# Kernel optimization log

Measured on AMD Instinct MI355X. Metric: run time of the kernel, lower is better.

The kernel has to match this reference:

```python
import jax, jax.numpy as jnp
import numpy as np
import math

B, N, HORIZON, E = 16, 4096, 12, 16
IN_DIM = HORIZON * E            # 192
T_DIM, H, D = 64, 4, 16         # transformer_dim, heads, head_dim
K_ORD = 3
FFN = 128
OUT_DIM = HORIZON * 16          # horizon * dim_out = 192
LN_EPS = 1e-5


def setup_inputs() -> dict:
    key = jax.random.key(0)
    ks = jax.random.split(key, 16)
    s = 0.02
    return {
        "x": jax.random.normal(ks[0], (B, N, IN_DIM), jnp.float32),
        "Wq": jax.random.normal(ks[1], (IN_DIM, T_DIM), jnp.float32) * s,
        "bq": jnp.zeros((T_DIM,), jnp.float32),
        "Wk": jax.random.normal(ks[2], (IN_DIM, T_DIM), jnp.float32) * s,
        "bk": jnp.zeros((T_DIM,), jnp.float32),
        "Wv": jax.random.normal(ks[3], (IN_DIM, T_DIM), jnp.float32) * s,
        "bv": jnp.zeros((T_DIM,), jnp.float32),
        "Win": jax.random.normal(ks[4], (IN_DIM, T_DIM), jnp.float32) * s,  # no bias
        "Wout": jax.random.normal(ks[5], (T_DIM, OUT_DIM), jnp.float32) * s,
        "bout": jnp.zeros((OUT_DIM,), jnp.float32),
        "W1": jax.random.normal(ks[6], (T_DIM, FFN), jnp.float32) * s,
        "b1": jnp.zeros((FFN,), jnp.float32),
        "W2": jax.random.normal(ks[7], (FFN, T_DIM), jnp.float32) * s,
        "b2": jnp.zeros((T_DIM,), jnp.float32),
        "ln_g": jnp.ones((T_DIM,), jnp.float32),
        "ln_b": jnp.zeros((T_DIM,), jnp.float32),
        "weights_pool": jax.random.normal(ks[8], (IN_DIM, OUT_DIM), jnp.float32) * s,
        "Pi": jax.random.normal(ks[9], (H, K_ORD + 1), jnp.float32) * 0.5,
    }


def _layer_norm(y, g, b):
    mu = jnp.mean(y, axis=-1, keepdims=True)
    var = jnp.mean((y - mu) ** 2, axis=-1, keepdims=True)
    return (y - mu) * jax.lax.rsqrt(var + LN_EPS) * g + b


def reference(x, Wq, bq, Wk, bk, Wv, bv, Win, Wout, bout,
              W1, b1, W2, b2, ln_g, ln_b, weights_pool, Pi):
    Bx, Nx, _ = x.shape
    # projections -> (B, H, N, d)
    Q = (x @ Wq + bq).reshape(Bx, Nx, H, D).transpose(0, 2, 1, 3)
    Kt = (x @ Wk + bk).reshape(Bx, Nx, H, D).transpose(0, 2, 1, 3)
    V = (x @ Wv + bv).reshape(Bx, Nx, H, D).transpose(0, 2, 1, 3)

    weighted_sum = jnp.zeros((Bx, H, Nx, D), x.dtype)
    for k in range(K_ORD + 1):
        if k == 0:
            # transform(0, .) returns ones with feature dim 1
            Qk = jnp.ones((Bx, H, Nx, 1), x.dtype)
            Kk = jnp.ones((Bx, H, Nx, 1), x.dtype)
        else:
            Qk = Q ** k   # elementwise power (exp-by-squaring == x**k)
            Kk = Kt ** k
        dk = Qk.shape[-1]
        # f_kv: (B,H,f,d) ; sumN: (B,H,f,1)
        f_kv = jnp.einsum('bhnf,bhnc->bhfc', Kk, V)
        sumN = jnp.sum(Kk, axis=2)[..., None]
        f_kv_norm = f_kv / (sumN + 1e-8) / math.sqrt(dk)
        c_k = jnp.einsum('bhnf,bhfc->bhnc', Qk, f_kv_norm)
        weighted_sum = weighted_sum + c_k * Pi[:, k][None, :, None, None]

    # NOTE: faithful to original: raw view of (B,H,N,d) as (B,N,H*d), no permute
    attention_out = weighted_sum.reshape(Bx, Nx, H * D) / math.factorial(K_ORD)

    proj = x @ Win
    res = _layer_norm(proj + attention_out, ln_g, ln_b)
    ffn = jax.nn.relu(res @ W1 + b1) @ W2 + b2   # dropout = identity (eval)
    res = _layer_norm(res + ffn, ln_g, ln_b)

    x_g = jnp.einsum('bni,io->bno', x, weights_pool)
    out = res @ Wout + bout
    return x_g + out
```

## Files before the change

kernel.cpp:

```cpp
#include <hip/hip_runtime.h>

typedef unsigned int u32;
typedef unsigned short u16;

#define NB 16
#define NN 4096
#define IND 192

typedef __attribute__((ext_vector_type(8))) short short8;
typedef __attribute__((ext_vector_type(4))) float f32x4;
#define MFMA16 __builtin_amdgcn_mfma_f32_16x16x32_bf16

__device__ __forceinline__ float bf2f(u16 u) {
  union { u32 i; float f; } c; c.i = ((u32)u) << 16; return c.f;
}
__device__ __forceinline__ float lo16(u32 u) {
  union { u32 i; float f; } c; c.i = u << 16; return c.f;
}
__device__ __forceinline__ float hi16(u32 u) {
  union { u32 i; float f; } c; c.i = u & 0xffff0000u; return c.f;
}
__device__ __forceinline__ u16 f2bf(float f) {
  union { float f; u32 i; } c; c.f = f;
  u32 r = c.i + 0x7fffu + ((c.i >> 16) & 1u);
  return (u16)(r >> 16);
}
__device__ __forceinline__ float ldwf(const void* p, int i, int isf) {
  return isf ? ((const float*)p)[i] : bf2f(((const u16*)p)[i]);
}
__device__ __forceinline__ short8 ld_frag8(const u16* p) {
  union { uint4 u; short8 s; } c;
  c.u = *reinterpret_cast<const uint4*>(p);
  return c.s;
}
__device__ __forceinline__ short8 as_short8(uint4 u) {
  union { uint4 u; short8 s; } c; c.u = u; return c.s;
}
__device__ __forceinline__ short8 pack8(const float* v) {
  short8 s;
  #pragma unroll
  for (int e = 0; e < 8; ++e) s[e] = (short)f2bf(v[e]);
  return s;
}
__device__ __forceinline__ float ln64(float y, float g, float be) {
  float s = y, sq = y * y;
  #pragma unroll
  for (int off = 32; off > 0; off >>= 1) {
    s  += __shfl_xor(s, off, 64);
    sq += __shfl_xor(sq, off, 64);
  }
  float mu  = s * 0.015625f;
  float var = sq * 0.015625f - mu * mu;
  return (y - mu) * rsqrtf(var + 1e-5f) * g + be;
}

__global__ __launch_bounds__(64) void k_detect(const u32* __restrict__ x2,
                                               int* __restrict__ flag) {
  int t = threadIdx.x;
  int bad = 0;
  for (int i = 0; i < 16; ++i) {
    float a = fabsf(lo16(x2[t * 16 + i]));
    if (!(a < 1e4f)) bad = 1;
  }
  int anybad = __any(bad);
  if (t == 0) *flag = anybad ? 1 : 0;
}

__global__ __launch_bounds__(256) void k_xb(const int* __restrict__ flag,
                                            const void* __restrict__ x,
                                            u16* __restrict__ xb) {
  const int isf = *flag;
  size_t gid = (size_t)blockIdx.x * 256 + threadIdx.x;
  if (isf) {
    const float4* src = (const float4*)x;
    for (size_t i = gid; i < 3145728; i += 1048576) {
      float4 v = src[i];
      ushort4 o;
      o.x = f2bf(v.x); o.y = f2bf(v.y); o.z = f2bf(v.z); o.w = f2bf(v.w);
      ((ushort4*)xb)[i] = o;
    }
  } else {
    const uint4* src = (const uint4*)x;
    for (size_t i = gid; i < 1572864; i += 1048576)
      ((uint4*)xb)[i] = src[i];
  }
}

__global__ __launch_bounds__(192) void k_xsum(const int* __restrict__ flag,
                                              const void* __restrict__ x,
                                              float* __restrict__ xsum) {
  const int isf = *flag;
  const int t = threadIdx.x;
  const int r0 = blockIdx.x * 256;
  const int b = r0 >> 12;
  float s = 0.f;
  if (isf) {
    const float* xp = (const float*)x;
    for (int r = 0; r < 256; ++r) s += xp[(size_t)(r0 + r) * 192 + t];
  } else {
    const u16* xp = (const u16*)x;
    for (int r = 0; r < 256; ++r) s += bf2f(xp[(size_t)(r0 + r) * 192 + t]);
  }
  atomicAdd(xsum + b * 192 + t, s);
}

__global__ __launch_bounds__(256) void k_prepw(
    const int* __restrict__ flag,
    const void* Wq, const void* Wk, const void* Wv, const void* Win,
    const void* Wout, const void* Wp, const void* W1, const void* W2,
    const void* bq, const void* bk, const void* bv,
    u16* __restrict__ Bs1, u16* __restrict__ BsKlo, u16* __restrict__ Bs2,
    u16* __restrict__ W1f, u16* __restrict__ W2f, float* __restrict__ bcat)
{
  const int isf = *flag;
  int idx = blockIdx.x * 256 + threadIdx.x;
  if (idx < 49152) {
    int e = idx & 7, l = (idx >> 3) & 63, g = idx >> 9;
    int nt = g & 15, ks = g >> 4;
    int k = ks * 32 + (l >> 4) * 8 + e;
    int n = nt * 16 + (l & 15);
    const void* W = (n < 64) ? Wq : (n < 128) ? Wk : (n < 192) ? Wv : Win;
    Bs1[idx] = f2bf(ldwf(W, k * 64 + (n & 63), isf));
  } else if (idx < 61440) {
    int j = idx - 49152;
    int e = j & 7, l = (j >> 3) & 63, g = j >> 9;
    int ntp = g & 3, ks = g >> 2;
    int k = ks * 32 + (l >> 4) * 8 + e;
    int n = ntp * 16 + (l & 15);
    float wv = ldwf(Wk, k * 64 + n, isf);
    u16 hi = f2bf(wv);
    BsKlo[j] = f2bf(wv - bf2f(hi));
  } else if (idx < 110592) {
    int j = idx - 61440;
    int e = j & 7, l = (j >> 3) & 63, g = j >> 9;
    int nt = g % 12, ks = g / 12;
    int k = ks * 32 + (l >> 4) * 8 + e;
    int n = nt * 16 + (l & 15);
    float v = (k < 64) ? ldwf(Wout, k * 192 + n, isf)
                       : ldwf(Wp, (k - 64) * 192 + n, isf);
    Bs2[j] = f2bf(v);
  } else if (idx < 118784) {
    int j = idx - 110592;
    int e = j & 7, l = (j >> 3) & 63, g = j >> 9;
    int nt = g & 7, ks = g >> 3;
    int k = ks * 32 + (l >> 4) * 8 + e;
    int n = nt * 16 + (l & 15);
    W1f[j] = f2bf(ldwf(W1, k * 128 + n, isf));
  } else if (idx < 126976) {
    int j = idx - 118784;
    int e = j & 7, l = (j >> 3) & 63, g = j >> 9;
    int nt = g & 3, ks = g >> 2;
    int k = ks * 32 + (l >> 4) * 8 + e;
    int n = nt * 16 + (l & 15);
    W2f[j] = f2bf(ldwf(W2, k * 64 + n, isf));
  } else if (idx < 127232) {
    int n = idx - 126976;
    bcat[n] = (n < 64)  ? ldwf(bq, n, isf)
            : (n < 128) ? ldwf(bk, n - 64, isf)
            : (n < 192) ? ldwf(bv, n - 128, isf) : 0.f;
  }
}

template<bool F32>
__device__ void gemm1_body(const void* __restrict__ x,
                           const u16* __restrict__ Bs1,
                           const u16* __restrict__ BsKlo,
                           const float* __restrict__ bcat,
                           u16* __restrict__ C1, float* __restrict__ stats,
                           float (*xs)[196], float (*Ks)[65], float (*Vs)[65])
{
  const int tid = threadIdx.x;
  const int mbase = blockIdx.x * 32;
  const int b = mbase >> 12;

  if constexpr (F32) {
    for (int i = tid; i < 1536; i += 512) {
      int row = i / 48, c4 = i - row * 48;
      float4 v = *((const float4*)x + (size_t)(mbase + row) * 48 + c4);
      *(float4*)&xs[row][c4 * 4] = v;
    }
  } else {
    for (int i = tid; i < 768; i += 512) {
      int row = i / 24, c8 = i - row * 24;
      uint4 v = *((const uint4*)x + (size_t)(mbase + row) * 24 + c8);
      float* dst = &xs[row][c8 * 8];
      dst[0]=lo16(v.x); dst[1]=hi16(v.x); dst[2]=lo16(v.y); dst[3]=hi16(v.y);
      dst[4]=lo16(v.z); dst[5]=hi16(v.z); dst[6]=lo16(v.w); dst[7]=hi16(v.w);
    }
  }
  __syncthreads();

  const int w = tid >> 6, l = tid & 63, lm = l & 15, lk = l >> 4;
  const int nt0 = w * 2;
  const bool isK = (w == 2) || (w == 3);

  short8 bhi[2][6], blo[2][6];
  #pragma unroll
  for (int n2 = 0; n2 < 2; ++n2)
    #pragma unroll
    for (int ks = 0; ks < 6; ++ks) {
      bhi[n2][ks] = ld_frag8(Bs1 + (size_t)((ks * 16 + nt0 + n2) * 64 + l) * 8);
      if (F32 && isK)
        blo[n2][ks] = ld_frag8(BsKlo + (size_t)((ks * 4 + nt0 + n2 - 4) * 64 + l) * 8);
    }
  float bias[2];
  bias[0] = bcat[nt0 * 16 + lm];
  bias[1] = bcat[(nt0 + 1) * 16 + lm];

  for (int mt = 0; mt < 2; ++mt) {
    short8 ahi[6], alo[6];
    const float* xr = &xs[mt * 16 + lm][0];
    #pragma unroll
    for (int ks = 0; ks < 6; ++ks) {
      float v[8];
      *(float4*)&v[0] = *(const float4*)(xr + ks * 32 + lk * 8);
      *(float4*)&v[4] = *(const float4*)(xr + ks * 32 + lk * 8 + 4);
      short8 h8;
      #pragma unroll
      for (int e = 0; e < 8; ++e) h8[e] = (short)f2bf(v[e]);
      ahi[ks] = h8;
      if (F32 && isK) {
        short8 l8;
        #pragma unroll
        for (int e = 0; e < 8; ++e) {
          float r = v[e] - bf2f((u16)h8[e]);
          l8[e] = (short)f2bf(r);
        }
        alo[ks] = l8;
      }
    }
    f32x4 acc[2];
    #pragma unroll
    for (int n2 = 0; n2 < 2; ++n2) {
      f32x4 a = {bias[n2], bias[n2], bias[n2], bias[n2]};
      acc[n2] = a;
    }
    #pragma unroll
    for (int ks = 0; ks < 6; ++ks)
      #pragma unroll
      for (int n2 = 0; n2 < 2; ++n2) {
        acc[n2] = MFMA16(ahi[ks], bhi[n2][ks], acc[n2], 0, 0, 0);
        if (F32 && isK) {
          acc[n2] = MFMA16(ahi[ks], blo[n2][ks], acc[n2], 0, 0, 0);
          acc[n2] = MFMA16(alo[ks], bhi[n2][ks], acc[n2], 0, 0, 0);
          acc[n2] = MFMA16(alo[ks], blo[n2][ks], acc[n2], 0, 0, 0);
        }
      }
    const int rl = mt * 16 + lk * 4;
    if (w < 2) {
      #pragma unroll
      for (int n2 = 0; n2 < 2; ++n2)
        #pragma unroll
        for (int r = 0; r < 4; ++r)
          C1[(size_t)(mbase + rl + r) * 128 + (nt0 + n2) * 16 + lm] = f2bf(acc[n2][r]);
    } else if (isK) {
      #pragma unroll
      for (int n2 = 0; n2 < 2; ++n2)
        #pragma unroll
        for (int r = 0; r < 4; ++r)
          Ks[rl + r][(nt0 + n2 - 4) * 16 + lm] = acc[n2][r];
    } else if (w < 6) {
      #pragma unroll
      for (int n2 = 0; n2 < 2; ++n2)
        #pragma unroll
        for (int r = 0; r < 4; ++r)
          Vs[rl + r][(nt0 + n2 - 8) * 16 + lm] = acc[n2][r];
    } else {
      #pragma unroll
      for (int n2 = 0; n2 < 2; ++n2)
        #pragma unroll
        for (int r = 0; r < 4; ++r)
          C1[(size_t)(mbase + rl + r) * 128 + 64 + (nt0 + n2 - 12) * 16 + lm] = f2bf(acc[n2][r]);
    }
  }
  __syncthreads();

  float* sb = stats + (size_t)(b * 4) * 832;
  #pragma unroll
  for (int it = 0; it < 2; ++it) {
    int item = tid + it * 512;
    int hh = item >> 8, f = (item >> 4) & 15, c = item & 15;
    float a1 = 0.f, a2 = 0.f, a3 = 0.f;
    for (int r = 0; r < 32; ++r) {
      float kv = Ks[r][hh * 16 + f];
      float vv = Vs[r][hh * 16 + c];
      float k2 = kv * kv;
      a1 = fmaf(kv, vv, a1);
      a2 = fmaf(k2, vv, a2);
      a3 = fmaf(k2 * kv, vv, a3);
    }
    float* base = sb + (size_t)hh * 832 + f * 16 + c;
    atomicAdd(base, a1);
    atomicAdd(base + 256, a2);
    atomicAdd(base + 512, a3);
  }
  if (tid < 192) {
    int kk = tid >> 6, hf = tid & 63, h2 = hf >> 4, ff = hf & 15;
    float s = 0.f;
    for (int r = 0; r < 32; ++r) {
      float kv = Ks[r][hf];
      s += (kk == 0) ? kv : (kk == 1) ? kv * kv : kv * kv * kv;
    }
    atomicAdd(sb + (size_t)h2 * 832 + 768 + kk * 16 + ff, s);
  } else if (tid < 256) {
    int hf = tid - 192, h2 = hf >> 4;
    float s = 0.f;
    for (int r = 0; r < 32; ++r) s += Vs[r][hf];
    atomicAdd(sb + (size_t)h2 * 832 + 816 + (hf & 15), s);
  }
}

__global__ __launch_bounds__(512, 2) void k_gemm1(
    const int* __restrict__ flag, const void* __restrict__ x,
    const u16* __restrict__ Bs1, const u16* __restrict__ BsKlo,
    const float* __restrict__ bcat,
    u16* __restrict__ C1, float* __restrict__ stats)
{
  __shared__ float xs[32][196];
  __shared__ float Ks[32][65];
  __shared__ float Vs[32][65];
  if (*flag) gemm1_body<true >(x, Bs1, BsKlo, bcat, C1, stats, xs, Ks, Vs);
  else       gemm1_body<false>(x, Bs1, BsKlo, bcat, C1, stats, xs, Ks, Vs);
}

template<bool F32>
__device__ void finalize_body(const float* stats, const void* Pi,
                              const void* Wk, const void* bk,
                              const float* xsum, float* M, float* sn1)
{
  const int bh = blockIdx.x, bb = bh >> 2, h = bh & 3, t = threadIdx.x;
  const float* sb = stats + (size_t)bh * 832;
  float* mb = M + (size_t)bh * 784;
  const float inv6 = 1.0f / 6.0f;

  {
    int f = t >> 4, s = t & 15;
    float p = 0.f;
    for (int i = s * 12; i < s * 12 + 12; ++i)
      p += xsum[bb * 192 + i] * ldwf(Wk, i * 64 + h * 16 + f, F32);
    p += __shfl_xor(p, 1, 64);
    p += __shfl_xor(p, 2, 64);
    p += __shfl_xor(p, 4, 64);
    p += __shfl_xor(p, 8, 64);
    if (s == 0) sn1[f] = p + 4096.0f * ldwf(bk, h * 16 + f, F32);
  }
  __syncthreads();

  {
    const int f = t >> 4, c = t & 15;
    #pragma unroll
    for (int k = 0; k < 3; ++k) {
      float fkv = sb[k * 256 + f * 16 + c];
      float sk  = (k == 0) ? sn1[f] : sb[768 + k * 16 + f];
      float pi  = ldwf(Pi, h * 4 + (k + 1), F32);
      mb[k * 256 + f * 16 + c] = fkv / ((sk + 1e-8f) * 4.0f) * pi * inv6;
    }
  }
  if (t < 16) {
    float sv  = sb[816 + t];
    float pi0 = ldwf(Pi, h * 4 + 0, F32);
    mb[768 + t] = sv / (4096.0f + 1e-8f) * pi0 * inv6;
  }
}

__global__ __launch_bounds__(256) void k_finalize(
    const int* __restrict__ flag, const float* __restrict__ stats,
    const void* __restrict__ Pi, const void* __restrict__ Wk,
    const void* __restrict__ bk, const float* __restrict__ xsum,
    float* __restrict__ M)
{
  __shared__ float sn1[16];
  if (*flag) finalize_body<true >(stats, Pi, Wk, bk, xsum, M, sn1);
  else       finalize_body<false>(stats, Pi, Wk, bk, xsum, M, sn1);
}

template<bool F32> __device__ void mid_body(
    const u16* __restrict__ C1, u16* __restrict__ R2,
    const float* __restrict__ Mall,
    const u16* __restrict__ W1f, const u16* __restrict__ W2f,
    const void* __restrict__ b1, const void* __restrict__ b2,
    const void* __restrict__ lng, const void* __restrict__ lnb,
    float (*attL)[72], u16 (*resB)[72], u16 (*hB)[136])
{
  const int tid = threadIdx.x;
  const int w = tid >> 6, l = tid & 63;
  const int lm = l & 15, lk = l >> 4;
  const int n0g = blockIdx.x * 64;
  const int b = n0g >> 12;
  const int n2_0 = n0g & 4095;
  const int h = n2_0 >> 10;
  const int qg0 = (b << 12) + ((n2_0 & 1023) << 2);
  const float* mb = Mall + (size_t)((b << 2) + h) * 784;

  short8 Bhi[2], Blo[2];
  #pragma unroll
  for (int ks = 0; ks < 2; ++ks) {
    float vh[8], vl[8];
    #pragma unroll
    for (int e = 0; e < 8; ++e) {
      int kk = ks * 32 + lk * 8 + e;
      float v = (kk < 16) ? mb[kk * 16 + lm]
              : (kk < 32) ? mb[256 + (kk - 16) * 16 + lm]
              : (kk < 48) ? mb[512 + (kk - 32) * 16 + lm] : 0.f;
      float hi = bf2f(f2bf(v));
      vh[e] = hi; vl[e] = v - hi;
    }
    Bhi[ks] = pack8(vh);
    Blo[ks] = pack8(vl);
  }
  const float c0v = mb[768 + lm];

  #pragma unroll
  for (int mt2 = 0; mt2 < 4; ++mt2) {
    const int mt = w * 4 + mt2;
    uint4 qv = *(const uint4*)(C1 + (size_t)(qg0 + mt * 16 + lm) * 128
                               + h * 16 + (lk & 1) * 8);
    float q[8] = {lo16(qv.x), hi16(qv.x), lo16(qv.y), hi16(qv.y),
                  lo16(qv.z), hi16(qv.z), lo16(qv.w), hi16(qv.w)};
    float q2[8], q3[8];
    #pragma unroll
    for (int e = 0; e < 8; ++e) { q2[e] = q[e] * q[e]; q3[e] = q2[e] * q[e]; }
    short8 a1, a2;
    if (lk < 2) { a1 = as_short8(qv); a2 = pack8(q3); }
    else        { a1 = pack8(q2);     a2 = short8{0,0,0,0,0,0,0,0}; }

    f32x4 acc = {c0v, c0v, c0v, c0v};
    acc = MFMA16(a1, Bhi[0], acc, 0, 0, 0);
    acc = MFMA16(a1, Blo[0], acc, 0, 0, 0);
    acc = MFMA16(a2, Bhi[1], acc, 0, 0, 0);
    acc = MFMA16(a2, Blo[1], acc, 0, 0, 0);

    #pragma unroll
    for (int r = 0; r < 4; ++r) {
      int qr = mt * 16 + lk * 4 + r;
      attL[qr >> 2][(qr & 3) * 16 + lm] = acc[r];
    }
  }

  const float gj = ldwf(lng, l, F32), bj = ldwf(lnb, l, F32);
  #pragma unroll 4
  for (int rr = 0; rr < 16; ++rr) {
    int r = w * 16 + rr;
    float proj = bf2f(C1[(size_t)(n0g + r) * 128 + 64 + l]);
    float y = proj + attL[r][l];
    resB[r][l] = f2bf(ln64(y, gj, bj));
  }

  short8 a0 = *(const short8*)&resB[w * 16 + lm][lk * 8];
  short8 a1f = *(const short8*)&resB[w * 16 + lm][32 + lk * 8];
  f32x4 hacc[8];
  #pragma unroll
  for (int nt = 0; nt < 8; ++nt) {
    float bv = ldwf(b1, nt * 16 + lm, F32);
    f32x4 a = {bv, bv, bv, bv};
    hacc[nt] = a;
  }
  #pragma unroll
  for (int nt = 0; nt < 8; ++nt) {
    short8 w1a = ld_frag8(W1f + (size_t)((0 * 8 + nt) * 64 + l) * 8);
    short8 w1b = ld_frag8(W1f + (size_t)((1 * 8 + nt) * 64 + l) * 8);
    hacc[nt] = MFMA16(a0, w1a, hacc[nt], 0, 0, 0);
    hacc[nt] = MFMA16(a1f, w1b, hacc[nt], 0, 0, 0);
  }
  #pragma unroll
  for (int nt = 0; nt < 8; ++nt)
    #pragma unroll
    for (int r = 0; r < 4; ++r) {
      int row = w * 16 + lk * 4 + r;
      hB[row][nt * 16 + lm] = f2bf(fmaxf(hacc[nt][r], 0.f));
    }

  short8 ha[4];
  #pragma unroll
  for (int ks = 0; ks < 4; ++ks)
    ha[ks] = *(const short8*)&hB[w * 16 + lm][ks * 32 + lk * 8];
  f32x4 oacc[4];
  #pragma unroll
  for (int nt = 0; nt < 4; ++nt) {
    float bv = ldwf(b2, nt * 16 + lm, F32);
    f32x4 a = {bv, bv, bv, bv};
    oacc[nt] = a;
  }
  #pragma unroll
  for (int ks = 0; ks < 4; ++ks)
    #pragma unroll
    for (int nt = 0; nt < 4; ++nt) {
      short8 w2v = ld_frag8(W2f + (size_t)((ks * 4 + nt) * 64 + l) * 8);
      oacc[nt] = MFMA16(ha[ks], w2v, oacc[nt], 0, 0, 0);
    }

  float gcol[4], bcol[4];
  #pragma unroll
  for (int nt = 0; nt < 4; ++nt) {
    gcol[nt] = ldwf(lng, nt * 16 + lm, F32);
    bcol[nt] = ldwf(lnb, nt * 16 + lm, F32);
  }
  #pragma unroll
  for (int r = 0; r < 4; ++r) {
    int row = w * 16 + lk * 4 + r;
    float y[4];
    float s = 0.f, sq = 0.f;
    #pragma unroll
    for (int nt = 0; nt < 4; ++nt) {
      y[nt] = oacc[nt][r] + bf2f(resB[row][nt * 16 + lm]);
      s += y[nt];
      sq = fmaf(y[nt], y[nt], sq);
    }
    #pragma unroll
    for (int off = 8; off > 0; off >>= 1) {
      s  += __shfl_xor(s, off, 64);
      sq += __shfl_xor(sq, off, 64);
    }
    float mu = s * 0.015625f;
    float var = sq * 0.015625f - mu * mu;
    float rs = rsqrtf(var + 1e-5f);
    #pragma unroll
    for (int nt = 0; nt < 4; ++nt) {
      float r2v = (y[nt] - mu) * rs * gcol[nt] + bcol[nt];
      R2[(size_t)(n0g + row) * 64 + nt * 16 + lm] = f2bf(r2v);
    }
  }
}

__global__ __launch_bounds__(256, 2) void k_mid(
    const int* __restrict__ flag, const u16* __restrict__ C1,
    u16* __restrict__ R2, const float* __restrict__ Mall,
    const u16* __restrict__ W1f, const u16* __restrict__ W2f,
    const void* __restrict__ b1, const void* __restrict__ b2,
    const void* __restrict__ lng, const void* __restrict__ lnb)
{
  __shared__ float attL[64][72];
  __shared__ u16 resB[64][72];
  __shared__ u16 hB[64][136];
  if (*flag) mid_body<true >(C1, R2, Mall, W1f, W2f, b1, b2, lng, lnb, attL, resB, hB);
  else       mid_body<false>(C1, R2, Mall, W1f, W2f, b1, b2, lng, lnb, attL, resB, hB);
}

__global__ __launch_bounds__(256, 2) void k_gemm2(
    const int* __restrict__ flag,
    const u16* __restrict__ R2, const u16* __restrict__ xb,
    const u16* __restrict__ Bs2, const void* __restrict__ bout,
    void* __restrict__ out)
{
  const int isf = *flag;
  const int l = threadIdx.x & 63;
  const int w = threadIdx.x >> 6;
  const int mbase = blockIdx.x * 64;
  const int lm = l & 15, lk = l >> 4;

  short8 bf[8][3];
  #pragma unroll
  for (int ks = 0; ks < 8; ++ks)
    #pragma unroll
    for (int nt = 0; nt < 3; ++nt)
      bf[ks][nt] = ld_frag8(Bs2 + (size_t)((ks * 12 + w * 3 + nt) * 64 + l) * 8);

  float bias[3];
  #pragma unroll
  for (int nt = 0; nt < 3; ++nt) bias[nt] = ldwf(bout, w * 48 + nt * 16 + lm, isf);

  short8 af[8];
  {
    const int row = mbase + lm;
    const u16* rp = R2 + (size_t)row * 64 + lk * 8;
    af[0] = ld_frag8(rp);
    af[1] = ld_frag8(rp + 32);
    const u16* xp = xb + (size_t)row * IND + lk * 8;
    #pragma unroll
    for (int ks = 2; ks < 8; ++ks) af[ks] = ld_frag8(xp + (ks - 2) * 32);
  }

  for (int mt = 0; mt < 4; ++mt) {
    short8 afn[8];
    if (mt < 3) {
      const int row = mbase + (mt + 1) * 16 + lm;
      const u16* rp = R2 + (size_t)row * 64 + lk * 8;
      afn[0] = ld_frag8(rp);
      afn[1] = ld_frag8(rp + 32);
      const u16* xp = xb + (size_t)row * IND + lk * 8;
      #pragma unroll
      for (int ks = 2; ks < 8; ++ks) afn[ks] = ld_frag8(xp + (ks - 2) * 32);
    }
    f32x4 acc[3];
    #pragma unroll
    for (int nt = 0; nt < 3; ++nt) {
      f32x4 a = {bias[nt], bias[nt], bias[nt], bias[nt]};
      acc[nt] = a;
    }
    #pragma unroll
    for (int ks = 0; ks < 8; ++ks)
      #pragma unroll
      for (int nt = 0; nt < 3; ++nt)
        acc[nt] = MFMA16(af[ks], bf[ks][nt], acc[nt], 0, 0, 0);
    const int r0 = mbase + mt * 16 + lk * 4;
    const int c0 = w * 48 + lm;
    if (isf) {
      float* op = (float*)out;
      #pragma unroll
      for (int nt = 0; nt < 3; ++nt)
        #pragma unroll
        for (int r = 0; r < 4; ++r)
          op[(size_t)(r0 + r) * IND + c0 + nt * 16] = acc[nt][r];
    } else {
      u16* op = (u16*)out;
      #pragma unroll
      for (int nt = 0; nt < 3; ++nt)
        #pragma unroll
        for (int r = 0; r < 4; ++r)
          op[(size_t)(r0 + r) * IND + c0 + nt * 16] = f2bf(acc[nt][r]);
    }
    #pragma unroll
    for (int ks = 0; ks < 8; ++ks) af[ks] = afn[ks];
  }
}

extern "C" void kernel_launch(void* const* d_in, const int* in_sizes, int n_in,
                              void* d_out, int out_size, void* d_ws, size_t ws_size,
                              hipStream_t stream)
{
  const void* x   = d_in[0];
  const void* Wq  = d_in[1];
  const void* bq  = d_in[2];
  const void* Wk  = d_in[3];
  const void* bk  = d_in[4];
  const void* Wv  = d_in[5];
  const void* bv  = d_in[6];
  const void* Win = d_in[7];
  const void* Wout= d_in[8];
  const void* bout= d_in[9];
  const void* W1  = d_in[10];
  const void* b1  = d_in[11];
  const void* W2  = d_in[12];
  const void* b2  = d_in[13];
  const void* lng = d_in[14];
  const void* lnb = d_in[15];
  const void* Wp  = d_in[16];
  const void* Pi  = d_in[17];

  u16* xb    = (u16*)d_ws;
  u16* C1    = xb + (size_t)12582912;
  u16* R2    = C1 + (size_t)8388608;
  u16* Bs1   = R2 + (size_t)4194304;
  u16* BsKlo = Bs1 + 49152;
  u16* Bs2   = BsKlo + 12288;
  u16* W1f   = Bs2 + 49152;
  u16* W2f   = W1f + 8192;
  float* bcat  = (float*)(W2f + 8192);
  float* stats = bcat + 256;
  float* xsum  = stats + 53248;
  float* Mc    = xsum + 3072;
  int*   flag  = (int*)(Mc + 50176);

  k_detect<<<1, 64, 0, stream>>>((const u32*)x, flag);
  hipMemsetAsync(stats, 0, (size_t)(53248 + 3072) * sizeof(float), stream);

  k_prepw<<<497, 256, 0, stream>>>(flag, Wq, Wk, Wv, Win, Wout, Wp, W1, W2,
                                   bq, bk, bv, Bs1, BsKlo, Bs2, W1f, W2f, bcat);
  k_xb<<<4096, 256, 0, stream>>>(flag, x, xb);
  k_xsum<<<256, 192, 0, stream>>>(flag, x, xsum);
  k_gemm1<<<2048, 512, 0, stream>>>(flag, x, Bs1, BsKlo, bcat, C1, stats);
  k_finalize<<<64, 256, 0, stream>>>(flag, stats, Pi, Wk, bk, xsum, Mc);
  k_mid<<<1024, 256, 0, stream>>>(flag, C1, R2, Mc, W1f, W2f, b1, b2, lng, lnb);
  k_gemm2<<<1024, 256, 0, stream>>>(flag, R2, xb, Bs2, bout, d_out);
}
```

Before: 161.5 us.

## Drop bf16 staging of x and restructure gemm1 with per-wave projection tiles

Removes the k_xb pass that wrote a bf16 copy of x; gemm1 and gemm2 now read x directly from global memory and convert fp32 to bf16 in registers. gemm1 is reorganised to 256 threads and 64 rows per block. Each wave computes one projection group with a block-rotated assignment, reading B fragments from global memory instead of holding them in registers, and the K-path error correction drops its lo*lo term. The K^kV statistics are register-blocked 4x4 per lane with shuffle reductions before fewer atomics, and k_xsum gets more, smaller blocks. This trades an extra full pass over x for re-reading fp32 x in gemm2 and repeated B-fragment loads.

```diff
diff --git a/kernel.cpp b/kernel.cpp
--- a/kernel.cpp
+++ b/kernel.cpp
@@ -16,9 +16,6 @@
 }
 __device__ __forceinline__ float lo16(u32 u) {
   union { u32 i; float f; } c; c.i = u << 16; return c.f;
-}
-__device__ __forceinline__ float hi16(u32 u) {
-  union { u32 i; float f; } c; c.i = u & 0xffff0000u; return c.f;
 }
 __device__ __forceinline__ u16 f2bf(float f) {
   union { float f; u32 i; } c; c.f = f;
@@ -33,15 +30,6 @@
   c.u = *reinterpret_cast<const uint4*>(p);
   return c.s;
 }
-__device__ __forceinline__ short8 as_short8(uint4 u) {
-  union { uint4 u; short8 s; } c; c.u = u; return c.s;
-}
-__device__ __forceinline__ short8 pack8(const float* v) {
-  short8 s;
-  #pragma unroll
-  for (int e = 0; e < 8; ++e) s[e] = (short)f2bf(v[e]);
-  return s;
-}
 __device__ __forceinline__ float ln64(float y, float g, float be) {
   float s = y, sq = y * y;
   #pragma unroll
@@ -52,6 +40,18 @@
   float mu  = s * 0.015625f;
   float var = sq * 0.015625f - mu * mu;
   return (y - mu) * rsqrtf(var + 1e-5f) * g + be;
+}
+__device__ __forceinline__ short8 pack8(const float* v) {
+  short8 s;
+  #pragma unroll
+  for (int e = 0; e < 8; ++e) s[e] = (short)f2bf(v[e]);
+  return s;
+}
+__device__ __forceinline__ short8 as_short8(uint4 u) {
+  union { uint4 u; short8 s; } c; c.u = u; return c.s;
+}
+__device__ __forceinline__ float hi16(u32 u) {
+  union { u32 i; float f; } c; c.i = u & 0xffff0000u; return c.f;
 }
 
 __global__ __launch_bounds__(64) void k_detect(const u32* __restrict__ x2,
@@ -66,40 +66,20 @@
   if (t == 0) *flag = anybad ? 1 : 0;
 }
 
-__global__ __launch_bounds__(256) void k_xb(const int* __restrict__ flag,
-                                            const void* __restrict__ x,
-                                            u16* __restrict__ xb) {
-  const int isf = *flag;
-  size_t gid = (size_t)blockIdx.x * 256 + threadIdx.x;
-  if (isf) {
-    const float4* src = (const float4*)x;
-    for (size_t i = gid; i < 3145728; i += 1048576) {
-      float4 v = src[i];
-      ushort4 o;
-      o.x = f2bf(v.x); o.y = f2bf(v.y); o.z = f2bf(v.z); o.w = f2bf(v.w);
-      ((ushort4*)xb)[i] = o;
-    }
-  } else {
-    const uint4* src = (const uint4*)x;
-    for (size_t i = gid; i < 1572864; i += 1048576)
-      ((uint4*)xb)[i] = src[i];
-  }
-}
-
 __global__ __launch_bounds__(192) void k_xsum(const int* __restrict__ flag,
                                               const void* __restrict__ x,
                                               float* __restrict__ xsum) {
   const int isf = *flag;
   const int t = threadIdx.x;
-  const int r0 = blockIdx.x * 256;
+  const int r0 = blockIdx.x * 64;
   const int b = r0 >> 12;
   float s = 0.f;
   if (isf) {
-    const float* xp = (const float*)x;
-    for (int r = 0; r < 256; ++r) s += xp[(size_t)(r0 + r) * 192 + t];
+    const float* xp = (const float*)x + (size_t)r0 * 192 + t;
+    for (int r = 0; r < 64; ++r) s += xp[(size_t)r * 192];
   } else {
-    const u16* xp = (const u16*)x;
-    for (int r = 0; r < 256; ++r) s += bf2f(xp[(size_t)(r0 + r) * 192 + t]);
+    const u16* xp = (const u16*)x + (size_t)r0 * 192 + t;
+    for (int r = 0; r < 64; ++r) s += bf2f(xp[(size_t)r * 192]);
   }
   atomicAdd(xsum + b * 192 + t, s);
 }
@@ -167,160 +147,171 @@
                            const u16* __restrict__ BsKlo,
                            const float* __restrict__ bcat,
                            u16* __restrict__ C1, float* __restrict__ stats,
-                           float (*xs)[196], float (*Ks)[65], float (*Vs)[65])
+                           float (*Ks)[68], float (*Vs)[68])
 {
   const int tid = threadIdx.x;
-  const int mbase = blockIdx.x * 32;
+  const int ww = tid >> 6, l = tid & 63;
+  const int lm = l & 15, lk = l >> 4;
+  const int mbase = blockIdx.x * 64;
   const int b = mbase >> 12;
-
-  if constexpr (F32) {
-    for (int i = tid; i < 1536; i += 512) {
-      int row = i / 48, c4 = i - row * 48;
-      float4 v = *((const float4*)x + (size_t)(mbase + row) * 48 + c4);
-      *(float4*)&xs[row][c4 * 4] = v;
-    }
-  } else {
-    for (int i = tid; i < 768; i += 512) {
-      int row = i / 24, c8 = i - row * 24;
-      uint4 v = *((const uint4*)x + (size_t)(mbase + row) * 24 + c8);
-      float* dst = &xs[row][c8 * 8];
-      dst[0]=lo16(v.x); dst[1]=hi16(v.x); dst[2]=lo16(v.y); dst[3]=hi16(v.y);
-      dst[4]=lo16(v.z); dst[5]=hi16(v.z); dst[6]=lo16(v.w); dst[7]=hi16(v.w);
-    }
-  }
-  __syncthreads();
-
-  const int w = tid >> 6, l = tid & 63, lm = l & 15, lk = l >> 4;
-  const int nt0 = w * 2;
-  const bool isK = (w == 2) || (w == 3);
-
-  short8 bhi[2][6], blo[2][6];
-  #pragma unroll
-  for (int n2 = 0; n2 < 2; ++n2)
-    #pragma unroll
-    for (int ks = 0; ks < 6; ++ks) {
-      bhi[n2][ks] = ld_frag8(Bs1 + (size_t)((ks * 16 + nt0 + n2) * 64 + l) * 8);
-      if (F32 && isK)
-        blo[n2][ks] = ld_frag8(BsKlo + (size_t)((ks * 4 + nt0 + n2 - 4) * 64 + l) * 8);
-    }
-  float bias[2];
-  bias[0] = bcat[nt0 * 16 + lm];
-  bias[1] = bcat[(nt0 + 1) * 16 + lm];
-
-  for (int mt = 0; mt < 2; ++mt) {
+  const int type = (ww + blockIdx.x) & 3;
+  const int nt0 = type * 4;
+  const bool isK = (type == 1);
+
+  float bias4[4];
+  #pragma unroll
+  for (int nt4 = 0; nt4 < 4; ++nt4) bias4[nt4] = bcat[(nt0 + nt4) * 16 + lm];
+
+  for (int mt = 0; mt < 4; ++mt) {
+    const int rowg = mbase + mt * 16 + lm;
     short8 ahi[6], alo[6];
-    const float* xr = &xs[mt * 16 + lm][0];
-    #pragma unroll
-    for (int ks = 0; ks < 6; ++ks) {
-      float v[8];
-      *(float4*)&v[0] = *(const float4*)(xr + ks * 32 + lk * 8);
-      *(float4*)&v[4] = *(const float4*)(xr + ks * 32 + lk * 8 + 4);
-      short8 h8;
-      #pragma unroll
-      for (int e = 0; e < 8; ++e) h8[e] = (short)f2bf(v[e]);
-      ahi[ks] = h8;
-      if (F32 && isK) {
-        short8 l8;
+    if constexpr (F32) {
+      const float* xr = (const float*)x + (size_t)rowg * 192 + lk * 8;
+      #pragma unroll
+      for (int ks = 0; ks < 6; ++ks) {
+        float v[8];
+        *(float4*)&v[0] = *(const float4*)(xr + ks * 32);
+        *(float4*)&v[4] = *(const float4*)(xr + ks * 32 + 4);
+        short8 h8;
         #pragma unroll
-        for (int e = 0; e < 8; ++e) {
-          float r = v[e] - bf2f((u16)h8[e]);
-          l8[e] = (short)f2bf(r);
-        }
-        alo[ks] = l8;
-      }
-    }
-    f32x4 acc[2];
-    #pragma unroll
-    for (int n2 = 0; n2 < 2; ++n2) {
-      f32x4 a = {bias[n2], bias[n2], bias[n2], bias[n2]};
-      acc[n2] = a;
-    }
-    #pragma unroll
-    for (int ks = 0; ks < 6; ++ks)
-      #pragma unroll
-      for (int n2 = 0; n2 < 2; ++n2) {
-        acc[n2] = MFMA16(ahi[ks], bhi[n2][ks], acc[n2], 0, 0, 0);
-        if (F32 && isK) {
-          acc[n2] = MFMA16(ahi[ks], blo[n2][ks], acc[n2], 0, 0, 0);
-          acc[n2] = MFMA16(alo[ks], bhi[n2][ks], acc[n2], 0, 0, 0);
-          acc[n2] = MFMA16(alo[ks], blo[n2][ks], acc[n2], 0, 0, 0);
+        for (int e = 0; e < 8; ++e) h8[e] = (short)f2bf(v[e]);
+        ahi[ks] = h8;
+        if (isK) {
+          short8 l8;
+          #pragma unroll
+          for (int e = 0; e < 8; ++e) l8[e] = (short)f2bf(v[e] - bf2f((u16)h8[e]));
+          alo[ks] = l8;
         }
       }
-    const int rl = mt * 16 + lk * 4;
-    if (w < 2) {
-      #pragma unroll
-      for (int n2 = 0; n2 < 2; ++n2)
+    } else {
+      const u16* xr = (const u16*)x + (size_t)rowg * 192 + lk * 8;
+      #pragma unroll
+      for (int ks = 0; ks < 6; ++ks) ahi[ks] = ld_frag8(xr + ks * 32);
+    }
+
+    #pragma unroll
+    for (int nt4 = 0; nt4 < 4; ++nt4) {
+      const int nt = nt0 + nt4;
+      const float bv = bias4[nt4];
+      f32x4 acc = {bv, bv, bv, bv};
+      #pragma unroll
+      for (int ks = 0; ks < 6; ++ks) {
+        short8 bhi = ld_frag8(Bs1 + (size_t)((ks * 16 + nt) * 64 + l) * 8);
+        acc = MFMA16(ahi[ks], bhi, acc, 0, 0, 0);
+        if (F32 && isK) {
+          short8 blo = ld_frag8(BsKlo + (size_t)((ks * 4 + nt4) * 64 + l) * 8);
+          acc = MFMA16(ahi[ks], blo, acc, 0, 0, 0);
+          acc = MFMA16(alo[ks], bhi, acc, 0, 0, 0);
+        }
+      }
+      const int rl = mt * 16 + lk * 4;
+      if (type == 0) {
         #pragma unroll
         for (int r = 0; r < 4; ++r)
-          C1[(size_t)(mbase + rl + r) * 128 + (nt0 + n2) * 16 + lm] = f2bf(acc[n2][r]);
-    } else if (isK) {
-      #pragma unroll
-      for (int n2 = 0; n2 < 2; ++n2)
+          C1[(size_t)(mbase + rl + r) * 128 + nt4 * 16 + lm] = f2bf(acc[r]);
+      } else if (type == 1) {
+        #pragma unroll
+        for (int r = 0; r < 4; ++r) Ks[rl + r][nt4 * 16 + lm] = acc[r];
+      } else if (type == 2) {
+        #pragma unroll
+        for (int r = 0; r < 4; ++r) Vs[rl + r][nt4 * 16 + lm] = acc[r];
+      } else {
         #pragma unroll
         for (int r = 0; r < 4; ++r)
-          Ks[rl + r][(nt0 + n2 - 4) * 16 + lm] = acc[n2][r];
-    } else if (w < 6) {
-      #pragma unroll
-      for (int n2 = 0; n2 < 2; ++n2)
-        #pragma unroll
-        for (int r = 0; r < 4; ++r)
-          Vs[rl + r][(nt0 + n2 - 8) * 16 + lm] = acc[n2][r];
-    } else {
-      #pragma unroll
-      for (int n2 = 0; n2 < 2; ++n2)
-        #pragma unroll
-        for (int r = 0; r < 4; ++r)
-          C1[(size_t)(mbase + rl + r) * 128 + 64 + (nt0 + n2 - 12) * 16 + lm] = f2bf(acc[n2][r]);
+          C1[(size_t)(mbase + rl + r) * 128 + 64 + nt4 * 16 + lm] = f2bf(acc[r]);
+      }
     }
   }
   __syncthreads();
 
-  float* sb = stats + (size_t)(b * 4) * 832;
-  #pragma unroll
-  for (int it = 0; it < 2; ++it) {
-    int item = tid + it * 512;
-    int hh = item >> 8, f = (item >> 4) & 15, c = item & 15;
-    float a1 = 0.f, a2 = 0.f, a3 = 0.f;
-    for (int r = 0; r < 32; ++r) {
-      float kv = Ks[r][hh * 16 + f];
-      float vv = Vs[r][hh * 16 + c];
-      float k2 = kv * kv;
-      a1 = fmaf(kv, vv, a1);
-      a2 = fmaf(k2, vv, a2);
-      a3 = fmaf(k2 * kv, vv, a3);
-    }
-    float* base = sb + (size_t)hh * 832 + f * 16 + c;
-    atomicAdd(base, a1);
-    atomicAdd(base + 256, a2);
-    atomicAdd(base + 512, a3);
-  }
-  if (tid < 192) {
-    int kk = tid >> 6, hf = tid & 63, h2 = hf >> 4, ff = hf & 15;
-    float s = 0.f;
-    for (int r = 0; r < 32; ++r) {
-      float kv = Ks[r][hf];
-      s += (kk == 0) ? kv : (kk == 1) ? kv * kv : kv * kv * kv;
-    }
-    atomicAdd(sb + (size_t)h2 * 832 + 768 + kk * 16 + ff, s);
-  } else if (tid < 256) {
-    int hf = tid - 192, h2 = hf >> 4;
-    float s = 0.f;
-    for (int r = 0; r < 32; ++r) s += Vs[r][hf];
-    atomicAdd(sb + (size_t)h2 * 832 + 816 + (hf & 15), s);
-  }
-}
-
-__global__ __launch_bounds__(512, 2) void k_gemm1(
+  const int h = ww;
+  const int fg = l & 3, cg = (l >> 2) & 3, rs = l >> 4;
+  float a1[4][4], a2[4][4], a3[4][4];
+  #pragma unroll
+  for (int fi = 0; fi < 4; ++fi)
+    #pragma unroll
+    for (int ci = 0; ci < 4; ++ci) { a1[fi][ci] = 0.f; a2[fi][ci] = 0.f; a3[fi][ci] = 0.f; }
+  float s2[4] = {0.f,0.f,0.f,0.f}, s3[4] = {0.f,0.f,0.f,0.f}, sv[4] = {0.f,0.f,0.f,0.f};
+
+  #pragma unroll 4
+  for (int j = 0; j < 16; ++j) {
+    const int r = rs * 16 + j;
+    float4 kq = *(const float4*)&Ks[r][h * 16 + fg * 4];
+    float4 vq = *(const float4*)&Vs[r][h * 16 + cg * 4];
+    float kv[4] = {kq.x, kq.y, kq.z, kq.w};
+    float vv[4] = {vq.x, vq.y, vq.z, vq.w};
+    float k2[4], k3[4];
+    #pragma unroll
+    for (int fi = 0; fi < 4; ++fi) { k2[fi] = kv[fi] * kv[fi]; k3[fi] = k2[fi] * kv[fi]; }
+    #pragma unroll
+    for (int fi = 0; fi < 4; ++fi)
+      #pragma unroll
+      for (int ci = 0; ci < 4; ++ci) {
+        a1[fi][ci] = fmaf(kv[fi], vv[ci], a1[fi][ci]);
+        a2[fi][ci] = fmaf(k2[fi], vv[ci], a2[fi][ci]);
+        a3[fi][ci] = fmaf(k3[fi], vv[ci], a3[fi][ci]);
+      }
+    if (cg == 0) {
+      #pragma unroll
+      for (int fi = 0; fi < 4; ++fi) { s2[fi] += k2[fi]; s3[fi] += k3[fi]; }
+    }
+    if (fg == 0) {
+      #pragma unroll
+      for (int ci = 0; ci < 4; ++ci) sv[ci] += vv[ci];
+    }
+  }
+  #pragma unroll
+  for (int fi = 0; fi < 4; ++fi)
+    #pragma unroll
+    for (int ci = 0; ci < 4; ++ci) {
+      a1[fi][ci] += __shfl_xor(a1[fi][ci], 16, 64);
+      a1[fi][ci] += __shfl_xor(a1[fi][ci], 32, 64);
+      a2[fi][ci] += __shfl_xor(a2[fi][ci], 16, 64);
+      a2[fi][ci] += __shfl_xor(a2[fi][ci], 32, 64);
+      a3[fi][ci] += __shfl_xor(a3[fi][ci], 16, 64);
+      a3[fi][ci] += __shfl_xor(a3[fi][ci], 32, 64);
+    }
+  #pragma unroll
+  for (int i = 0; i < 4; ++i) {
+    s2[i] += __shfl_xor(s2[i], 16, 64); s2[i] += __shfl_xor(s2[i], 32, 64);
+    s3[i] += __shfl_xor(s3[i], 16, 64); s3[i] += __shfl_xor(s3[i], 32, 64);
+    sv[i] += __shfl_xor(sv[i], 16, 64); sv[i] += __shfl_xor(sv[i], 32, 64);
+  }
+  if (rs == 0) {
+    float* sb = stats + (size_t)(b * 4 + h) * 832;
+    #pragma unroll
+    for (int fi = 0; fi < 4; ++fi)
+      #pragma unroll
+      for (int ci = 0; ci < 4; ++ci) {
+        const int off = (fg * 4 + fi) * 16 + cg * 4 + ci;
+        atomicAdd(sb + off, a1[fi][ci]);
+        atomicAdd(sb + 256 + off, a2[fi][ci]);
+        atomicAdd(sb + 512 + off, a3[fi][ci]);
+      }
+    if (cg == 0) {
+      #pragma unroll
+      for (int fi = 0; fi < 4; ++fi) {
+        atomicAdd(sb + 784 + fg * 4 + fi, s2[fi]);
+        atomicAdd(sb + 800 + fg * 4 + fi, s3[fi]);
+      }
+    }
+    if (fg == 0) {
+      #pragma unroll
+      for (int ci = 0; ci < 4; ++ci) atomicAdd(sb + 816 + cg * 4 + ci, sv[ci]);
+    }
+  }
+}
+
+__global__ __launch_bounds__(256, 3) void k_gemm1(
     const int* __restrict__ flag, const void* __restrict__ x,
     const u16* __restrict__ Bs1, const u16* __restrict__ BsKlo,
     const float* __restrict__ bcat,
     u16* __restrict__ C1, float* __restrict__ stats)
 {
-  __shared__ float xs[32][196];
-  __shared__ float Ks[32][65];
-  __shared__ float Vs[32][65];
-  if (*flag) gemm1_body<true >(x, Bs1, BsKlo, bcat, C1, stats, xs, Ks, Vs);
-  else       gemm1_body<false>(x, Bs1, BsKlo, bcat, C1, stats, xs, Ks, Vs);
+  __shared__ float Ks[64][68];
+  __shared__ float Vs[64][68];
+  if (*flag) gemm1_body<true >(x, Bs1, BsKlo, bcat, C1, stats, Ks, Vs);
+  else       gemm1_body<false>(x, Bs1, BsKlo, bcat, C1, stats, Ks, Vs);
 }
 
 template<bool F32>
@@ -438,6 +429,7 @@
   }
 
   const float gj = ldwf(lng, l, F32), bj = ldwf(lnb, l, F32);
+  float res1v[8]; (void)res1v;
   #pragma unroll 4
   for (int rr = 0; rr < 16; ++rr) {
     int r = w * 16 + rr;
@@ -536,13 +528,13 @@
   else       mid_body<false>(C1, R2, Mall, W1f, W2f, b1, b2, lng, lnb, attL, resB, hB);
 }
 
-__global__ __launch_bounds__(256, 2) void k_gemm2(
-    const int* __restrict__ flag,
-    const u16* __restrict__ R2, const u16* __restrict__ xb,
-    const u16* __restrict__ Bs2, const void* __restrict__ bout,
-    void* __restrict__ out)
-{
-  const int isf = *flag;
+template<bool F32>
+__device__ void gemm2_body(const void* __restrict__ x,
+                           const u16* __restrict__ R2,
+                           const u16* __restrict__ Bs2,
+                           const void* __restrict__ bout,
+                           void* __restrict__ out)
+{
   const int l = threadIdx.x & 63;
   const int w = threadIdx.x >> 6;
   const int mbase = blockIdx.x * 64;
@@ -557,30 +549,31 @@
 
   float bias[3];
   #pragma unroll
-  for (int nt = 0; nt < 3; ++nt) bias[nt] = ldwf(bout, w * 48 + nt * 16 + lm, isf);
-
-  short8 af[8];
-  {
-    const int row = mbase + lm;
-    const u16* rp = R2 + (size_t)row * 64 + lk * 8;
-    af[0] = ld_frag8(rp);
-    af[1] = ld_frag8(rp + 32);
-    const u16* xp = xb + (size_t)row * IND + lk * 8;
-    #pragma unroll
-    for (int ks = 2; ks < 8; ++ks) af[ks] = ld_frag8(xp + (ks - 2) * 32);
-  }
+  for (int nt = 0; nt < 3; ++nt) bias[nt] = ldwf(bout, w * 48 + nt * 16 + lm, F32);
 
   for (int mt = 0; mt < 4; ++mt) {
-    short8 afn[8];
-    if (mt < 3) {
-      const int row = mbase + (mt + 1) * 16 + lm;
+    const int row = mbase + mt * 16 + lm;
+    short8 af[8];
+    {
       const u16* rp = R2 + (size_t)row * 64 + lk * 8;
-      afn[0] = ld_frag8(rp);
-      afn[1] = ld_frag8(rp + 32);
-      const u16* xp = xb + (size_t)row * IND + lk * 8;
-      #pragma unroll
-      for (int ks = 2; ks < 8; ++ks) afn[ks] = ld_frag8(xp + (ks - 2) * 32);
-    }
+      af[0] = ld_frag8(rp);
+      af[1] = ld_frag8(rp + 32);
+    }
+    if constexpr (F32) {
+      const float* xp = (const float*)x + (size_t)row * 192 + lk * 8;
+      #pragma unroll
+      for (int ks = 2; ks < 8; ++ks) {
+        float v[8];
+        *(float4*)&v[0] = *(const float4*)(xp + (ks - 2) * 32);
+        *(float4*)&v[4] = *(const float4*)(xp + (ks - 2) * 32 + 4);
+        af[ks] = pack8(v);
+      }
+    } else {
+      const u16* xp = (const u16*)x + (size_t)row * 192 + lk * 8;
+      #pragma unroll
+      for (int ks = 2; ks < 8; ++ks) af[ks] = ld_frag8(xp + (ks - 2) * 32);
+    }
+
     f32x4 acc[3];
     #pragma unroll
     for (int nt = 0; nt < 3; ++nt) {
@@ -594,7 +587,7 @@
         acc[nt] = MFMA16(af[ks], bf[ks][nt], acc[nt], 0, 0, 0);
     const int r0 = mbase + mt * 16 + lk * 4;
     const int c0 = w * 48 + lm;
-    if (isf) {
+    if constexpr (F32) {
       float* op = (float*)out;
       #pragma unroll
       for (int nt = 0; nt < 3; ++nt)
@@ -609,9 +602,16 @@
         for (int r = 0; r < 4; ++r)
           op[(size_t)(r0 + r) * IND + c0 + nt * 16] = f2bf(acc[nt][r]);
     }
-    #pragma unroll
-    for (int ks = 0; ks < 8; ++ks) af[ks] = afn[ks];
-  }
+  }
+}
+
+__global__ __launch_bounds__(256, 2) void k_gemm2(
+    const int* __restrict__ flag, const void* __restrict__ x,
+    const u16* __restrict__ R2, const u16* __restrict__ Bs2,
+    const void* __restrict__ bout, void* __restrict__ out)
+{
+  if (*flag) gemm2_body<true >(x, R2, Bs2, bout, out);
+  else       gemm2_body<false>(x, R2, Bs2, bout, out);
 }
 
 extern "C" void kernel_launch(void* const* d_in, const int* in_sizes, int n_in,
@@ -637,8 +637,7 @@
   const void* Wp  = d_in[16];
   const void* Pi  = d_in[17];
 
-  u16* xb    = (u16*)d_ws;
-  u16* C1    = xb + (size_t)12582912;
+  u16* C1    = (u16*)d_ws;
   u16* R2    = C1 + (size_t)8388608;
   u16* Bs1   = R2 + (size_t)4194304;
   u16* BsKlo = Bs1 + 49152;
@@ -656,10 +655,9 @@
 
   k_prepw<<<497, 256, 0, stream>>>(flag, Wq, Wk, Wv, Win, Wout, Wp, W1, W2,
                                    bq, bk, bv, Bs1, BsKlo, Bs2, W1f, W2f, bcat);
-  k_xb<<<4096, 256, 0, stream>>>(flag, x, xb);
-  k_xsum<<<256, 192, 0, stream>>>(flag, x, xsum);
-  k_gemm1<<<2048, 512, 0, stream>>>(flag, x, Bs1, BsKlo, bcat, C1, stats);
+  k_xsum<<<1024, 192, 0, stream>>>(flag, x, xsum);
+  k_gemm1<<<1024, 256, 0, stream>>>(flag, x, Bs1, BsKlo, bcat, C1, stats);
   k_finalize<<<64, 256, 0, stream>>>(flag, stats, Pi, Wk, bk, xsum, Mc);
   k_mid<<<1024, 256, 0, stream>>>(flag, C1, R2, Mc, W1f, W2f, b1, b2, lng, lnb);
-  k_gemm2<<<1024, 256, 0, stream>>>(flag, R2, xb, Bs2, bout, d_out);
-}
+  k_gemm2<<<1024, 256, 0, stream>>>(flag, x, R2, Bs2, bout, d_out);
+}
```

Result: slower. 247.9 us (+53.5%).
